# Performance work log

Hardware: AMD Instinct MI355X
Metric: run time of the kernel (lower is better)

## Reference

```python
import jax, jax.numpy as jnp
import numpy as np

IN_CH = 128
HIDDEN = 256
CHUNK = 4096
EPS = 1e-8  # F.cosine_similarity default eps


def setup_inputs() -> dict:
    key = jax.random.key(0)
    ks = jax.random.split(key, 10)
    N, E, P = 8192, 262144, 65536
    x = jax.random.normal(ks[0], (N, IN_CH), dtype=jnp.float32)
    edge_index = jax.random.randint(ks[1], (2, E), 0, N, dtype=jnp.int64)
    edge_pairs = jax.random.randint(ks[2], (P, 2), 0, N, dtype=jnp.int64)
    input_dim = 2 * IN_CH + IN_CH + IN_CH + IN_CH + 1 + 3  # 644
    h2 = HIDDEN // 2
    def lin(k, fan_in, fan_out):
        bound = 1.0 / np.sqrt(fan_in)
        kw, kb = jax.random.split(k)
        W = jax.random.uniform(kw, (fan_in, fan_out), minval=-bound, maxval=bound, dtype=jnp.float32)
        b = jax.random.uniform(kb, (fan_out,), minval=-bound, maxval=bound, dtype=jnp.float32)
        return W, b
    W1, b1 = lin(ks[3], input_dim, HIDDEN)
    W2, b2 = lin(ks[4], HIDDEN, h2)
    W3, b3 = lin(ks[5], h2, 1)
    return {"x": x, "edge_index": edge_index, "edge_pairs": edge_pairs,
            "W1": W1, "b1": b1, "W2": W2, "b2": b2, "W3": W3, "b3": b3}


def _forward(x, edge_index, edge_pairs, W1, b1, W2, b2, W3, b3):
    N = x.shape[0]
    # dense adjacency cache (matches DenseHeuristicMixin._ensure_graph_cache)
    adj = jnp.zeros((N, N), dtype=jnp.float32).at[edge_index[0], edge_index[1]].set(1.0)
    diag = jnp.arange(N)
    adj = adj.at[diag, diag].set(0.0)
    deg = adj.sum(axis=1)
    inv_log_deg = jnp.where(deg > 1, 1.0 / jnp.log(jnp.where(deg > 1, deg, 2.0)), 0.0)
    inv_deg = jnp.where(deg > 0, 1.0 / jnp.where(deg > 0, deg, 1.0), 0.0)

    P = edge_pairs.shape[0]
    pairs = edge_pairs.reshape(P // CHUNK, CHUNK, 2)

    def chunk_body(carry, pc):
        u, v = pc[:, 0], pc[:, 1]
        xu, xv = x[u], x[v]                          # [C, d]
        # cosine similarity (eps-clamped denominator, as in torch)
        nu = jnp.sqrt(jnp.sum(xu * xu, axis=1))
        nv = jnp.sqrt(jnp.sum(xv * xv, axis=1))
        cos = jnp.sum(xu * xv, axis=1) / jnp.maximum(nu * nv, EPS)
        # dense heuristic features: [C, N] adjacency-row products
        common = adj[u] * adj[v]
        cn = common.sum(axis=1)
        aa = common @ inv_log_deg
        ra = common @ inv_deg
        feats = jnp.concatenate(
            [xu, xv, xu * xv, jnp.abs(xu - xv), xu + xv,
             cos[:, None], cn[:, None], aa[:, None], ra[:, None]], axis=1)
        h = jax.nn.relu(feats @ W1 + b1)  # dropout is identity in eval mode
        h = jax.nn.relu(h @ W2 + b2)
        s = (h @ W3 + b3)[:, 0]
        return carry, s

    _, scores = jax.lax.scan(chunk_body, None, pairs)
    return scores.reshape(-1)


def reference(x, edge_index, edge_pairs, W1, b1, W2, b2, W3, b3):
    return _forward(x, edge_index, edge_pairs, W1, b1, W2, b2, W3, b3)
```

## Files before the change

kernel.cpp:

```cpp
#include <hip/hip_runtime.h>
#include <hip/hip_bf16.h>

#define IN_CH   128
#define HIDDEN  256
#define H2DIM   128
#define KS1     17
#define KS2     8
#define NT1     16
#define NT2     8
#define FSTRIDE 552
#define H1S     264
#define H2S     136
#define H2OFF   16896
#define CAP     64
#define T1PACK  (NT1*KS1*64)
#define T2PACK  (NT2*KS2*64)

typedef short short8v __attribute__((ext_vector_type(8)));
typedef float f32x4   __attribute__((ext_vector_type(4)));

__device__ __forceinline__ ushort f2bf(float f) {
  union { float f; uint32_t u; } c; c.f = f;
  uint32_t u = c.u + 0x7FFFu + ((c.u >> 16) & 1u);
  return (ushort)(u >> 16);
}
__device__ __forceinline__ float bf2f(ushort h) {
  union { uint32_t u; float f; } c; c.u = ((uint32_t)h) << 16;
  return c.f;
}
__device__ __forceinline__ uint32_t pk2(float a, float b) {
  __hip_bfloat162 h = __float22bfloat162_rn(make_float2(a, b));
  union { __hip_bfloat162 h; uint32_t u; } c; c.h = h;
  return c.u;
}
__device__ __forceinline__ uint4 pack8(float4 lo, float4 hi) {
  uint4 r;
  r.x = pk2(lo.x, lo.y); r.y = pk2(lo.z, lo.w);
  r.z = pk2(hi.x, hi.y); r.w = pk2(hi.z, hi.w);
  return r;
}

__global__ void k_prep(const float* __restrict__ W1, const float* __restrict__ W2,
                       ushort* __restrict__ w1p, ushort* __restrict__ w2p,
                       uint32_t* __restrict__ bits, int nwords) {
  int t = blockIdx.x * blockDim.x + threadIdx.x;
  if (t < T1PACK) {
    int l = t & 63;
    int rest = t >> 6;
    int ks = rest % KS1;
    int nt = rest / KS1;
    int n  = nt * 16 + (l & 15);
    int k0 = ks * 32 + (l >> 4) * 8;
    short8v v;
    #pragma unroll
    for (int j = 0; j < 8; ++j) {
      int k = k0 + j;
      float val;
      if (k < 128)      val = W1[(size_t)k * HIDDEN + n] + W1[(size_t)(512 + k) * HIDDEN + n];
      else if (k < 256) val = W1[(size_t)k * HIDDEN + n] + W1[(size_t)(384 + k) * HIDDEN + n];
      else if (k < 512) val = W1[(size_t)k * HIDDEN + n];
      else if (k < 516) val = W1[(size_t)(k + 128) * HIDDEN + n];
      else              val = 0.f;
      v[j] = (short)f2bf(val);
    }
    *(short8v*)(w1p + (size_t)t * 8) = v;
  } else if (t < T1PACK + T2PACK) {
    int t2 = t - T1PACK;
    int l = t2 & 63;
    int rest = t2 >> 6;
    int ks = rest % KS2;
    int nt = rest / KS2;
    int n  = nt * 16 + (l & 15);
    int k0 = ks * 32 + (l >> 4) * 8;
    short8v v;
    #pragma unroll
    for (int j = 0; j < 8; ++j)
      v[j] = (short)f2bf(W2[(size_t)(k0 + j) * H2DIM + n]);
    *(short8v*)(w2p + (size_t)t2 * 8) = v;
  }
  int stride = gridDim.x * blockDim.x;
  for (int i = t; i < nwords; i += stride) bits[i] = 0u;
}

__global__ void k_build_adj(const int* __restrict__ ei, int E, int roww,
                            uint32_t* __restrict__ bits) {
  int e = blockIdx.x * blockDim.x + threadIdx.x;
  if (e >= E) return;
  int u = ei[e];
  int v = ei[E + e];
  if (u == v) return;
  atomicOr((unsigned int*)&bits[(size_t)u * roww + (v >> 5)], 1u << (v & 31));
}

__global__ void k_node_lists(const uint32_t* __restrict__ bits, const float* __restrict__ x,
                             int nnodes, int roww,
                             float* __restrict__ invlog, float* __restrict__ invdeg,
                             int* __restrict__ deg, float* __restrict__ nrm,
                             ushort* __restrict__ adjl) {
  int node = blockIdx.x * (blockDim.x >> 6) + (threadIdx.x >> 6);
  int lane = threadIdx.x & 63;
  if (node >= nnodes) return;
  const uint32_t* row = bits + (size_t)node * roww;
  uint32_t wd[4];
  int c = 0;
  #pragma unroll
  for (int j = 0; j < 4; ++j) { wd[j] = row[lane * 4 + j]; c += __popc(wd[j]); }
  int sum = c;
  #pragma unroll
  for (int off = 1; off < 64; off <<= 1) {
    int t = __shfl_up(sum, off);
    if (lane >= off) sum += t;
  }
  int excl = sum - c;
  int total = __shfl(sum, 63);
  ushort* lst = adjl + (size_t)node * CAP;
  int pos = excl;
  #pragma unroll
  for (int j = 0; j < 4; ++j) {
    uint32_t m = wd[j];
    int base = (lane * 4 + j) * 32;
    while (m) {
      int b = __ffs(m) - 1;
      if (pos < CAP) lst[pos] = (ushort)(base + b);
      ++pos;
      m &= m - 1;
    }
  }
  float2 xa = *(const float2*)(x + (size_t)node * IN_CH + 2 * lane);
  float ss = xa.x * xa.x + xa.y * xa.y;
  #pragma unroll
  for (int off = 32; off; off >>= 1) ss += __shfl_xor(ss, off);
  if (lane == 0) {
    deg[node] = total;
    float d = (float)total;
    invlog[node] = (total > 1) ? 1.0f / logf(d) : 0.0f;
    invdeg[node] = (total > 0) ? 1.0f / d : 0.0f;
    nrm[node] = sqrtf(ss);
  }
}

__global__ __launch_bounds__(512, 4) void k_mlp4(
    const float* __restrict__ x, const int* __restrict__ pairs,
    const uint32_t* __restrict__ bits, int roww,
    const int* __restrict__ deg, const float* __restrict__ nrm,
    const float* __restrict__ invlog, const float* __restrict__ invdeg,
    const ushort* __restrict__ adjl,
    const ushort* __restrict__ w1p, const float* __restrict__ b1,
    const ushort* __restrict__ w2p, const float* __restrict__ b2,
    const float* __restrict__ W3, const float* __restrict__ b3,
    float* __restrict__ out, int P)
{
  __shared__ ushort feats[64 * FSTRIDE];
  __shared__ int us[64], vs[64];

  int tid = threadIdx.x;
  int pb = blockIdx.x * 64;
  int w  = tid >> 6, l = tid & 63;

  if (tid < 64) {
    int2 pr = ((const int2*)pairs)[pb + tid];
    us[tid] = pr.x; vs[tid] = pr.y;
  }
  __syncthreads();

  {
    int pg = l >> 3, g = l & 7;
    int p = w * 8 + pg;
    int u = us[p], v = vs[p];
    const float* xu = x + (size_t)u * IN_CH + g * 16;
    const float* xv = x + (size_t)v * IN_CH + g * 16;
    float4 a0 = *(const float4*)(xu + 0),  a1 = *(const float4*)(xu + 4);
    float4 a2 = *(const float4*)(xu + 8),  a3 = *(const float4*)(xu + 12);
    float4 b0 = *(const float4*)(xv + 0),  b1v = *(const float4*)(xv + 4);
    float4 b2v = *(const float4*)(xv + 8), b3v = *(const float4*)(xv + 12);
    ushort* fpR = feats + p * FSTRIDE;
    ushort* fp  = fpR + g * 16;
    *(uint4*)(fp)       = pack8(a0, a1);
    *(uint4*)(fp + 8)   = pack8(a2, a3);
    *(uint4*)(fp + 128) = pack8(b0, b1v);
    *(uint4*)(fp + 136) = pack8(b2v, b3v);
    float4 c0, c1, c2, c3, d0, d1, d2, d3;
    c0.x=a0.x*b0.x;  c0.y=a0.y*b0.y;  c0.z=a0.z*b0.z;  c0.w=a0.w*b0.w;
    c1.x=a1.x*b1v.x; c1.y=a1.y*b1v.y; c1.z=a1.z*b1v.z; c1.w=a1.w*b1v.w;
    c2.x=a2.x*b2v.x; c2.y=a2.y*b2v.y; c2.z=a2.z*b2v.z; c2.w=a2.w*b2v.w;
    c3.x=a3.x*b3v.x; c3.y=a3.y*b3v.y; c3.z=a3.z*b3v.z; c3.w=a3.w*b3v.w;
    d0.x=fabsf(a0.x-b0.x);  d0.y=fabsf(a0.y-b0.y);  d0.z=fabsf(a0.z-b0.z);  d0.w=fabsf(a0.w-b0.w);
    d1.x=fabsf(a1.x-b1v.x); d1.y=fabsf(a1.y-b1v.y); d1.z=fabsf(a1.z-b1v.z); d1.w=fabsf(a1.w-b1v.w);
    d2.x=fabsf(a2.x-b2v.x); d2.y=fabsf(a2.y-b2v.y); d2.z=fabsf(a2.z-b2v.z); d2.w=fabsf(a2.w-b2v.w);
    d3.x=fabsf(a3.x-b3v.x); d3.y=fabsf(a3.y-b3v.y); d3.z=fabsf(a3.z-b3v.z); d3.w=fabsf(a3.w-b3v.w);
    *(uint4*)(fp + 256) = pack8(c0, c1);
    *(uint4*)(fp + 264) = pack8(c2, c3);
    *(uint4*)(fp + 384) = pack8(d0, d1);
    *(uint4*)(fp + 392) = pack8(d2, d3);
    float suv = c0.x+c0.y+c0.z+c0.w + c1.x+c1.y+c1.z+c1.w
              + c2.x+c2.y+c2.z+c2.w + c3.x+c3.y+c3.z+c3.w;
    suv += __shfl_xor(suv, 1);
    suv += __shfl_xor(suv, 2);
    suv += __shfl_xor(suv, 4);
    if (g == 0) {
      float cosv = suv / fmaxf(nrm[u] * nrm[v], 1e-8f);
      fpR[512] = f2bf(cosv);
    }
    if (g < 7) {
      *(uint32_t*)(fpR + 516 + 4 * g) = 0u;
      *(uint32_t*)(fpR + 516 + 4 * g + 2) = 0u;
    }
  }

  for (int pp = 0; pp < 8; ++pp) {
    int p = w * 8 + pp;
    int u = us[p], v = vs[p];
    int du = deg[u], dv = deg[v];
    int s_ = (du <= dv) ? u : v;
    int o_ = (du <= dv) ? v : u;
    int dmin = min(du, dv);
    float cnv, aa = 0.f, ra = 0.f;
    if (dmin <= CAP) {
      bool h = false; int nb = 0;
      if (l < dmin) {
        nb = adjl[(size_t)s_ * CAP + l];
        h = (bits[(size_t)o_ * roww + (nb >> 5)] >> (nb & 31)) & 1u;
      }
      unsigned long long mask = __ballot(h);
      cnv = (float)__popcll(mask);
      if (mask) {
        float il = 0.f, ig = 0.f;
        if (h) { il = invlog[nb]; ig = invdeg[nb]; }
        while (mask) {
          int ln = __ffsll(mask) - 1;
          aa += __shfl(il, ln);
          ra += __shfl(ig, ln);
          mask &= mask - 1;
        }
      }
    } else {
      float cnL = 0.f, aaL = 0.f, raL = 0.f;
      const uint32_t* ru = bits + (size_t)u * roww;
      const uint32_t* rv = bits + (size_t)v * roww;
      for (int wd = l; wd < roww; wd += 64) {
        uint32_t c = ru[wd] & rv[wd];
        cnL += (float)__popc(c);
        while (c) {
          int bb = __ffs(c) - 1;
          int idx = wd * 32 + bb;
          aaL += invlog[idx]; raL += invdeg[idx];
          c &= c - 1;
        }
      }
      #pragma unroll
      for (int off = 32; off; off >>= 1) {
        cnL += __shfl_xor(cnL, off);
        aaL += __shfl_xor(aaL, off);
        raL += __shfl_xor(raL, off);
      }
      cnv = cnL; aa = aaL; ra = raL;
    }
    if (l == 0) {
      ushort* fpR = feats + p * FSTRIDE;
      fpR[513] = f2bf(cnv);
      fpR[514] = f2bf(aa);
      fpR[515] = f2bf(ra);
    }
  }
  __syncthreads();

  int lr = l & 15;
  int lk = l >> 4;

  f32x4 acc[4][2];
  #pragma unroll
  for (int m = 0; m < 4; ++m)
    #pragma unroll
    for (int i = 0; i < 2; ++i) acc[m][i] = (f32x4){0.f, 0.f, 0.f, 0.f};

  const ushort* aB = feats + lr * FSTRIDE + lk * 8;
  const ushort* bW = w1p + (size_t)(w * 2) * KS1 * 512 + l * 8;

  short8v bf[2][2];
  #pragma unroll
  for (int i = 0; i < 2; ++i)
    bf[0][i] = *(const short8v*)(bW + (size_t)(i * KS1) * 512);

  #pragma unroll
  for (int ks = 0; ks < KS1; ++ks) {
    int cur = ks & 1, nxt = cur ^ 1;
    if (ks + 1 < KS1) {
      #pragma unroll
      for (int i = 0; i < 2; ++i)
        bf[nxt][i] = *(const short8v*)(bW + (size_t)(i * KS1 + ks + 1) * 512);
    }
    short8v am[4];
    #pragma unroll
    for (int m = 0; m < 4; ++m)
      am[m] = *(const short8v*)(aB + m * 16 * FSTRIDE + ks * 32);
    #pragma unroll
    for (int i = 0; i < 2; ++i)
      #pragma unroll
      for (int m = 0; m < 4; ++m)
        acc[m][i] = __builtin_amdgcn_mfma_f32_16x16x32_bf16(am[m], bf[cur][i], acc[m][i], 0, 0, 0);
  }

  uint32_t h1r[2][8];
  #pragma unroll
  for (int i = 0; i < 2; ++i) {
    float bias = b1[(w * 2 + i) * 16 + lr];
    #pragma unroll
    for (int m = 0; m < 4; ++m) {
      float v0 = fmaxf(acc[m][i][0] + bias, 0.f);
      float v1 = fmaxf(acc[m][i][1] + bias, 0.f);
      float v2 = fmaxf(acc[m][i][2] + bias, 0.f);
      float v3 = fmaxf(acc[m][i][3] + bias, 0.f);
      h1r[i][m * 2]     = pk2(v0, v1);
      h1r[i][m * 2 + 1] = pk2(v2, v3);
    }
  }
  __syncthreads();

  ushort* h1 = feats;
  #pragma unroll
  for (int i = 0; i < 2; ++i) {
    int col = (w * 2 + i) * 16 + lr;
    #pragma unroll
    for (int m = 0; m < 4; ++m) {
      int row0 = m * 16 + lk * 4;
      h1[(row0)     * H1S + col] = (ushort)(h1r[i][m * 2]);
      h1[(row0 + 1) * H1S + col] = (ushort)(h1r[i][m * 2] >> 16);
      h1[(row0 + 2) * H1S + col] = (ushort)(h1r[i][m * 2 + 1]);
      h1[(row0 + 3) * H1S + col] = (ushort)(h1r[i][m * 2 + 1] >> 16);
    }
  }
  __syncthreads();

  f32x4 acc2[4];
  #pragma unroll
  for (int m = 0; m < 4; ++m) acc2[m] = (f32x4){0.f, 0.f, 0.f, 0.f};

  const ushort* aB2 = h1 + lr * H1S + lk * 8;
  const ushort* bW2 = w2p + (size_t)w * KS2 * 512 + l * 8;

  short8v b2f[2];
  b2f[0] = *(const short8v*)(bW2);

  #pragma unroll
  for (int ks = 0; ks < KS2; ++ks) {
    int cur = ks & 1, nxt = cur ^ 1;
    if (ks + 1 < KS2)
      b2f[nxt] = *(const short8v*)(bW2 + (size_t)(ks + 1) * 512);
    #pragma unroll
    for (int m = 0; m < 4; ++m) {
      short8v am = *(const short8v*)(aB2 + m * 16 * H1S + ks * 32);
      acc2[m] = __builtin_amdgcn_mfma_f32_16x16x32_bf16(am, b2f[cur], acc2[m], 0, 0, 0);
    }
  }

  ushort* h2 = feats + H2OFF;
  {
    int col = w * 16 + lr;
    float bias = b2[col];
    #pragma unroll
    for (int m = 0; m < 4; ++m) {
      int row0 = m * 16 + lk * 4;
      #pragma unroll
      for (int r = 0; r < 4; ++r)
        h2[(row0 + r) * H2S + col] = f2bf(fmaxf(acc2[m][r] + bias, 0.f));
    }
  }
  __syncthreads();

  {
    int p = tid >> 3, g = tid & 7;
    const ushort* hp = h2 + p * H2S + g * 16;
    float s = 0.f;
    #pragma unroll
    for (int j = 0; j < 16; ++j) s += bf2f(hp[j]) * W3[g * 16 + j];
    s += __shfl_down(s, 4, 8);
    s += __shfl_down(s, 2, 8);
    s += __shfl_down(s, 1, 8);
    if (g == 0) out[pb + p] = s + b3[0];
  }
}

extern "C" void kernel_launch(void* const* d_in, const int* in_sizes, int n_in,
                              void* d_out, int out_size, void* d_ws, size_t ws_size,
                              hipStream_t stream) {
  const float* x     = (const float*)d_in[0];
  const int*   ei    = (const int*)d_in[1];
  const int*   pairs = (const int*)d_in[2];
  const float* W1    = (const float*)d_in[3];
  const float* b1    = (const float*)d_in[4];
  const float* W2    = (const float*)d_in[5];
  const float* b2    = (const float*)d_in[6];
  const float* W3    = (const float*)d_in[7];
  const float* b3    = (const float*)d_in[8];
  float* out = (float*)d_out;

  int N = in_sizes[0] / IN_CH;
  int E = in_sizes[1] / 2;
  int P = in_sizes[2] / 2;
  int roww = (N + 31) >> 5;

  char* wsb = (char*)d_ws;
  uint32_t* bits = (uint32_t*)wsb;                       size_t off = (size_t)N * roww * 4;
  float* invlog  = (float*)(wsb + off);                  off += (size_t)N * 4;
  float* invdeg  = (float*)(wsb + off);                  off += (size_t)N * 4;
  int*   deg     = (int*)(wsb + off);                    off += (size_t)N * 4;
  float* nrm     = (float*)(wsb + off);                  off += (size_t)N * 4;
  ushort* adjl   = (ushort*)(wsb + off);                 off += (size_t)N * CAP * 2;
  ushort* w1pack = (ushort*)(wsb + off);                 off += (size_t)T1PACK * 8 * 2;
  ushort* w2pack = (ushort*)(wsb + off);                 off += (size_t)T2PACK * 8 * 2;

  int nwords = N * roww;
  k_prep<<<1024, 256, 0, stream>>>(W1, W2, w1pack, w2pack, bits, nwords);
  k_build_adj<<<(E + 255) / 256, 256, 0, stream>>>(ei, E, roww, bits);
  k_node_lists<<<(N + 3) / 4, 256, 0, stream>>>(bits, x, N, roww, invlog, invdeg, deg, nrm, adjl);
  k_mlp4<<<P / 64, 512, 0, stream>>>(x, pairs, bits, roww, deg, nrm, invlog, invdeg, adjl,
                                     w1pack, b1, w2pack, b2, W3, b3, out, P);
}
```

Baseline: 81.33 us.

## Merge graph-prep kernels into cooperative kernel and batch heuristic loads

The prep, adjacency-build and node-list kernels become one cooperative kernel that separates its phases with grid-wide syncs, which removes two kernel launches and their gaps. In the MLP kernel, each wave now loads the pair indices, degrees, neighbour-list entries and adjacency bit words for all eight of its pairs before the common-neighbour computation, so these dependent global loads can overlap instead of running one pair at a time. The cost is extra registers per thread and grid.sync overhead, plus an all-or-nothing fallback to the slow bitmap path when any of a wave's eight pairs exceeds the list cap. Neighbour-list entries are also read regardless of degree, and the index is masked with 8191.

```diff
diff --git a/kernel.cpp b/kernel.cpp
--- a/kernel.cpp
+++ b/kernel.cpp
@@ -1,5 +1,8 @@
 #include <hip/hip_runtime.h>
 #include <hip/hip_bf16.h>
+#include <hip/hip_cooperative_groups.h>
+
+namespace cg = cooperative_groups;
 
 #define IN_CH   128
 #define HIDDEN  256
@@ -40,10 +43,20 @@
   return r;
 }
 
-__global__ void k_prep(const float* __restrict__ W1, const float* __restrict__ W2,
-                       ushort* __restrict__ w1p, ushort* __restrict__ w2p,
-                       uint32_t* __restrict__ bits, int nwords) {
+__global__ void k_graph(const float* __restrict__ x, const int* __restrict__ ei,
+                        const float* __restrict__ W1, const float* __restrict__ W2,
+                        ushort* __restrict__ w1p, ushort* __restrict__ w2p,
+                        uint32_t* __restrict__ bits,
+                        float* __restrict__ invlog, float* __restrict__ invdeg,
+                        int* __restrict__ deg, float* __restrict__ nrm,
+                        ushort* __restrict__ adjl,
+                        int N, int E, int roww, int nwords) {
+  cg::grid_group grid = cg::this_grid();
   int t = blockIdx.x * blockDim.x + threadIdx.x;
+  int nthr = gridDim.x * blockDim.x;
+
+  for (int i = t; i < nwords; i += nthr) bits[i] = 0u;
+
   if (t < T1PACK) {
     int l = t & 63;
     int rest = t >> 6;
@@ -78,68 +91,61 @@
       v[j] = (short)f2bf(W2[(size_t)(k0 + j) * H2DIM + n]);
     *(short8v*)(w2p + (size_t)t2 * 8) = v;
   }
-  int stride = gridDim.x * blockDim.x;
-  for (int i = t; i < nwords; i += stride) bits[i] = 0u;
-}
-
-__global__ void k_build_adj(const int* __restrict__ ei, int E, int roww,
-                            uint32_t* __restrict__ bits) {
-  int e = blockIdx.x * blockDim.x + threadIdx.x;
-  if (e >= E) return;
-  int u = ei[e];
-  int v = ei[E + e];
-  if (u == v) return;
-  atomicOr((unsigned int*)&bits[(size_t)u * roww + (v >> 5)], 1u << (v & 31));
-}
-
-__global__ void k_node_lists(const uint32_t* __restrict__ bits, const float* __restrict__ x,
-                             int nnodes, int roww,
-                             float* __restrict__ invlog, float* __restrict__ invdeg,
-                             int* __restrict__ deg, float* __restrict__ nrm,
-                             ushort* __restrict__ adjl) {
-  int node = blockIdx.x * (blockDim.x >> 6) + (threadIdx.x >> 6);
-  int lane = threadIdx.x & 63;
-  if (node >= nnodes) return;
-  const uint32_t* row = bits + (size_t)node * roww;
-  uint32_t wd[4];
-  int c = 0;
-  #pragma unroll
-  for (int j = 0; j < 4; ++j) { wd[j] = row[lane * 4 + j]; c += __popc(wd[j]); }
-  int sum = c;
-  #pragma unroll
-  for (int off = 1; off < 64; off <<= 1) {
-    int t = __shfl_up(sum, off);
-    if (lane >= off) sum += t;
-  }
-  int excl = sum - c;
-  int total = __shfl(sum, 63);
-  ushort* lst = adjl + (size_t)node * CAP;
-  int pos = excl;
-  #pragma unroll
-  for (int j = 0; j < 4; ++j) {
-    uint32_t m = wd[j];
-    int base = (lane * 4 + j) * 32;
-    while (m) {
-      int b = __ffs(m) - 1;
-      if (pos < CAP) lst[pos] = (ushort)(base + b);
-      ++pos;
-      m &= m - 1;
-    }
-  }
-  float2 xa = *(const float2*)(x + (size_t)node * IN_CH + 2 * lane);
-  float ss = xa.x * xa.x + xa.y * xa.y;
-  #pragma unroll
-  for (int off = 32; off; off >>= 1) ss += __shfl_xor(ss, off);
-  if (lane == 0) {
-    deg[node] = total;
-    float d = (float)total;
-    invlog[node] = (total > 1) ? 1.0f / logf(d) : 0.0f;
-    invdeg[node] = (total > 0) ? 1.0f / d : 0.0f;
-    nrm[node] = sqrtf(ss);
-  }
-}
-
-__global__ __launch_bounds__(512, 4) void k_mlp4(
+
+  grid.sync();
+
+  for (int e = t; e < E; e += nthr) {
+    int u = ei[e];
+    int v = ei[E + e];
+    if (u != v)
+      atomicOr((unsigned int*)&bits[(size_t)u * roww + (v >> 5)], 1u << (v & 31));
+  }
+
+  grid.sync();
+
+  int wid = t >> 6, lane = t & 63, nwaves = nthr >> 6;
+  for (int node = wid; node < N; node += nwaves) {
+    const uint32_t* row = bits + (size_t)node * roww;
+    uint32_t wd[4];
+    int c = 0;
+    #pragma unroll
+    for (int j = 0; j < 4; ++j) { wd[j] = row[lane * 4 + j]; c += __popc(wd[j]); }
+    int sum = c;
+    #pragma unroll
+    for (int off = 1; off < 64; off <<= 1) {
+      int tt = __shfl_up(sum, off);
+      if (lane >= off) sum += tt;
+    }
+    int excl = sum - c;
+    int total = __shfl(sum, 63);
+    ushort* lst = adjl + (size_t)node * CAP;
+    int pos = excl;
+    #pragma unroll
+    for (int j = 0; j < 4; ++j) {
+      uint32_t m = wd[j];
+      int base = (lane * 4 + j) * 32;
+      while (m) {
+        int b = __ffs(m) - 1;
+        if (pos < CAP) lst[pos] = (ushort)(base + b);
+        ++pos;
+        m &= m - 1;
+      }
+    }
+    float2 xa = *(const float2*)(x + (size_t)node * IN_CH + 2 * lane);
+    float ss = xa.x * xa.x + xa.y * xa.y;
+    #pragma unroll
+    for (int off = 32; off; off >>= 1) ss += __shfl_xor(ss, off);
+    if (lane == 0) {
+      deg[node] = total;
+      float d = (float)total;
+      invlog[node] = (total > 1) ? 1.0f / logf(d) : 0.0f;
+      invdeg[node] = (total > 0) ? 1.0f / d : 0.0f;
+      nrm[node] = sqrtf(ss);
+    }
+  }
+}
+
+__global__ __launch_bounds__(512, 4) void k_mlp5(
     const float* __restrict__ x, const int* __restrict__ pairs,
     const uint32_t* __restrict__ bits, int roww,
     const int* __restrict__ deg, const float* __restrict__ nrm,
@@ -162,6 +168,19 @@
     us[tid] = pr.x; vs[tid] = pr.y;
   }
   __syncthreads();
+
+  int pu[8], pv[8];
+  #pragma unroll
+  for (int pp = 0; pp < 8; ++pp) { pu[pp] = us[w * 8 + pp]; pv[pp] = vs[w * 8 + pp]; }
+  int du[8], dv[8];
+  #pragma unroll
+  for (int pp = 0; pp < 8; ++pp) { du[pp] = deg[pu[pp]]; dv[pp] = deg[pv[pp]]; }
+  int nbu[8], nbv[8];
+  #pragma unroll
+  for (int pp = 0; pp < 8; ++pp) {
+    nbu[pp] = adjl[(size_t)pu[pp] * CAP + l];
+    nbv[pp] = adjl[(size_t)pv[pp] * CAP + l];
+  }
 
   {
     int pg = l >> 3, g = l & 7;
@@ -207,59 +226,73 @@
     }
   }
 
-  for (int pp = 0; pp < 8; ++pp) {
-    int p = w * 8 + pp;
-    int u = us[p], v = vs[p];
-    int du = deg[u], dv = deg[v];
-    int s_ = (du <= dv) ? u : v;
-    int o_ = (du <= dv) ? v : u;
-    int dmin = min(du, dv);
-    float cnv, aa = 0.f, ra = 0.f;
-    if (dmin <= CAP) {
-      bool h = false; int nb = 0;
-      if (l < dmin) {
-        nb = adjl[(size_t)s_ * CAP + l];
-        h = (bits[(size_t)o_ * roww + (nb >> 5)] >> (nb & 31)) & 1u;
-      }
-      unsigned long long mask = __ballot(h);
-      cnv = (float)__popcll(mask);
-      if (mask) {
-        float il = 0.f, ig = 0.f;
-        if (h) { il = invlog[nb]; ig = invdeg[nb]; }
-        while (mask) {
-          int ln = __ffsll(mask) - 1;
-          aa += __shfl(il, ln);
-          ra += __shfl(ig, ln);
-          mask &= mask - 1;
+  {
+    int dmin[8], nbs[8];
+    uint32_t wrd[8];
+    bool fall = false;
+    #pragma unroll
+    for (int pp = 0; pp < 8; ++pp) {
+      bool ule = du[pp] <= dv[pp];
+      dmin[pp] = ule ? du[pp] : dv[pp];
+      int o   = ule ? pv[pp] : pu[pp];
+      int nb  = (ule ? nbu[pp] : nbv[pp]) & 8191;
+      nbs[pp] = nb;
+      wrd[pp] = bits[(size_t)o * roww + (nb >> 5)];
+      fall |= (dmin[pp] > CAP);
+    }
+    if (!fall) {
+      #pragma unroll
+      for (int pp = 0; pp < 8; ++pp) {
+        bool h = (l < dmin[pp]) && ((wrd[pp] >> (nbs[pp] & 31)) & 1u);
+        unsigned long long mask = __ballot(h);
+        float cnv = (float)__popcll(mask);
+        float aa = 0.f, ra = 0.f;
+        if (mask) {
+          float il = 0.f, ig = 0.f;
+          if (h) { il = invlog[nbs[pp]]; ig = invdeg[nbs[pp]]; }
+          while (mask) {
+            int ln = __ffsll(mask) - 1;
+            aa += __shfl(il, ln);
+            ra += __shfl(ig, ln);
+            mask &= mask - 1;
+          }
+        }
+        if (l == 0) {
+          ushort* fpR = feats + (w * 8 + pp) * FSTRIDE;
+          fpR[513] = f2bf(cnv);
+          fpR[514] = f2bf(aa);
+          fpR[515] = f2bf(ra);
         }
       }
     } else {
-      float cnL = 0.f, aaL = 0.f, raL = 0.f;
-      const uint32_t* ru = bits + (size_t)u * roww;
-      const uint32_t* rv = bits + (size_t)v * roww;
-      for (int wd = l; wd < roww; wd += 64) {
-        uint32_t c = ru[wd] & rv[wd];
-        cnL += (float)__popc(c);
-        while (c) {
-          int bb = __ffs(c) - 1;
-          int idx = wd * 32 + bb;
-          aaL += invlog[idx]; raL += invdeg[idx];
-          c &= c - 1;
+      for (int pp = 0; pp < 8; ++pp) {
+        int u = pu[pp], v = pv[pp];
+        float cnL = 0.f, aaL = 0.f, raL = 0.f;
+        const uint32_t* ru = bits + (size_t)u * roww;
+        const uint32_t* rv = bits + (size_t)v * roww;
+        for (int wd = l; wd < roww; wd += 64) {
+          uint32_t c = ru[wd] & rv[wd];
+          cnL += (float)__popc(c);
+          while (c) {
+            int bb = __ffs(c) - 1;
+            int idx = wd * 32 + bb;
+            aaL += invlog[idx]; raL += invdeg[idx];
+            c &= c - 1;
+          }
+        }
+        #pragma unroll
+        for (int off = 32; off; off >>= 1) {
+          cnL += __shfl_xor(cnL, off);
+          aaL += __shfl_xor(aaL, off);
+          raL += __shfl_xor(raL, off);
+        }
+        if (l == 0) {
+          ushort* fpR = feats + (w * 8 + pp) * FSTRIDE;
+          fpR[513] = f2bf(cnL);
+          fpR[514] = f2bf(aaL);
+          fpR[515] = f2bf(raL);
         }
       }
-      #pragma unroll
-      for (int off = 32; off; off >>= 1) {
-        cnL += __shfl_xor(cnL, off);
-        aaL += __shfl_xor(aaL, off);
-        raL += __shfl_xor(raL, off);
-      }
-      cnv = cnL; aa = aaL; ra = raL;
-    }
-    if (l == 0) {
-      ushort* fpR = feats + p * FSTRIDE;
-      fpR[513] = f2bf(cnv);
-      fpR[514] = f2bf(aa);
-      fpR[515] = f2bf(ra);
     }
   }
   __syncthreads();
@@ -410,9 +443,11 @@
   ushort* w2pack = (ushort*)(wsb + off);                 off += (size_t)T2PACK * 8 * 2;
 
   int nwords = N * roww;
-  k_prep<<<1024, 256, 0, stream>>>(W1, W2, w1pack, w2pack, bits, nwords);
-  k_build_adj<<<(E + 255) / 256, 256, 0, stream>>>(ei, E, roww, bits);
-  k_node_lists<<<(N + 3) / 4, 256, 0, stream>>>(bits, x, N, roww, invlog, invdeg, deg, nrm, adjl);
-  k_mlp4<<<P / 64, 512, 0, stream>>>(x, pairs, bits, roww, deg, nrm, invlog, invdeg, adjl,
+  void* gargs[] = { (void*)&x, (void*)&ei, (void*)&W1, (void*)&W2,
+                    (void*)&w1pack, (void*)&w2pack, (void*)&bits,
+                    (void*)&invlog, (void*)&invdeg, (void*)&deg, (void*)&nrm,
+                    (void*)&adjl, (void*)&N, (void*)&E, (void*)&roww, (void*)&nwords };
+  hipLaunchCooperativeKernel((void*)k_graph, dim3(1024), dim3(256), gargs, 0, stream);
+  k_mlp5<<<P / 64, 512, 0, stream>>>(x, pairs, bits, roww, deg, nrm, invlog, invdeg, adjl,
                                      w1pack, b1, w2pack, b2, W3, b3, out, P);
 }
```

Result: slower. 253.7 us (+212.0%).

## Halve feature LDS tile by splitting GEMM1 K into two passes, batch neighbor loads

Applied to the files above, without the earlier changes.

Shrinks the per-block shared feature buffer to about half by computing the first layer's K dimension in two passes. The first pass covers xu, xv, cos and the heuristics. Then xu*xv and |xu-xv| are recomputed from re-read x rows into the same buffer for the second pass. This is meant to let more blocks reside per CU (launch bounds raised to 8). Common-neighbor loads for all 8 pairs per wave are now issued up front to overlap latency. The final W3 dot product is fused into the layer-2 epilogue via shuffles and LDS atomics, removing the h2 staging buffer. The cost is extra global reads of x, additional barriers, and register pressure under the tighter occupancy bound.

```diff
diff --git a/kernel.cpp b/kernel.cpp
--- a/kernel.cpp
+++ b/kernel.cpp
@@ -8,10 +8,8 @@
 #define KS2     8
 #define NT1     16
 #define NT2     8
-#define FSTRIDE 552
+#define FSTR    296
 #define H1S     264
-#define H2S     136
-#define H2OFF   16896
 #define CAP     64
 #define T1PACK  (NT1*KS1*64)
 #define T2PACK  (NT2*KS2*64)
@@ -139,7 +137,7 @@
   }
 }
 
-__global__ __launch_bounds__(512, 4) void k_mlp4(
+__global__ __launch_bounds__(512, 8) void k_mlp7(
     const float* __restrict__ x, const int* __restrict__ pairs,
     const uint32_t* __restrict__ bits, int roww,
     const int* __restrict__ deg, const float* __restrict__ nrm,
@@ -150,35 +148,164 @@
     const float* __restrict__ W3, const float* __restrict__ b3,
     float* __restrict__ out, int P)
 {
-  __shared__ ushort feats[64 * FSTRIDE];
+  __shared__ ushort feats[64 * FSTR];
+  __shared__ float outacc[64];
   __shared__ int us[64], vs[64];
 
   int tid = threadIdx.x;
   int pb = blockIdx.x * 64;
   int w  = tid >> 6, l = tid & 63;
+  int pg = l >> 3, g = l & 7;
+  int lr = l & 15;
+  int lk = l >> 4;
 
   if (tid < 64) {
     int2 pr = ((const int2*)pairs)[pb + tid];
     us[tid] = pr.x; vs[tid] = pr.y;
-  }
-  __syncthreads();
-
-  {
-    int pg = l >> 3, g = l & 7;
-    int p = w * 8 + pg;
-    int u = us[p], v = vs[p];
-    const float* xu = x + (size_t)u * IN_CH + g * 16;
-    const float* xv = x + (size_t)v * IN_CH + g * 16;
+    outacc[tid] = b3[0];
+  }
+  __syncthreads();
+
+  int p = w * 8 + pg;
+  int u = us[p], v = vs[p];
+  const float* xu = x + (size_t)u * IN_CH + g * 16;
+  const float* xv = x + (size_t)v * IN_CH + g * 16;
+  ushort* fpR = feats + p * FSTR;
+  ushort* fp  = fpR + g * 16;
+
+  {
     float4 a0 = *(const float4*)(xu + 0),  a1 = *(const float4*)(xu + 4);
     float4 a2 = *(const float4*)(xu + 8),  a3 = *(const float4*)(xu + 12);
     float4 b0 = *(const float4*)(xv + 0),  b1v = *(const float4*)(xv + 4);
     float4 b2v = *(const float4*)(xv + 8), b3v = *(const float4*)(xv + 12);
-    ushort* fpR = feats + p * FSTRIDE;
-    ushort* fp  = fpR + g * 16;
     *(uint4*)(fp)       = pack8(a0, a1);
     *(uint4*)(fp + 8)   = pack8(a2, a3);
     *(uint4*)(fp + 128) = pack8(b0, b1v);
     *(uint4*)(fp + 136) = pack8(b2v, b3v);
+    float suv = a0.x*b0.x + a0.y*b0.y + a0.z*b0.z + a0.w*b0.w
+              + a1.x*b1v.x + a1.y*b1v.y + a1.z*b1v.z + a1.w*b1v.w
+              + a2.x*b2v.x + a2.y*b2v.y + a2.z*b2v.z + a2.w*b2v.w
+              + a3.x*b3v.x + a3.y*b3v.y + a3.z*b3v.z + a3.w*b3v.w;
+    suv += __shfl_xor(suv, 1);
+    suv += __shfl_xor(suv, 2);
+    suv += __shfl_xor(suv, 4);
+    if (g == 0) fpR[256] = f2bf(suv / fmaxf(nrm[u] * nrm[v], 1e-8f));
+    if (g < 7) *(uint2*)(fpR + 260 + 4 * g) = make_uint2(0u, 0u);
+  }
+
+  {
+    int sdmin[8], snbs[8];
+    uint32_t swrd[8];
+    bool sfall = false;
+    #pragma unroll
+    for (int pp = 0; pp < 8; ++pp) {
+      int ps_ = w * 8 + pp;
+      int uu = us[ps_], vv = vs[ps_];
+      int du = deg[uu], dv = deg[vv];
+      int nu = adjl[(size_t)uu * CAP + l];
+      int nv = adjl[(size_t)vv * CAP + l];
+      bool ule = du <= dv;
+      sdmin[pp] = ule ? du : dv;
+      int o  = ule ? vv : uu;
+      int nb = (ule ? nu : nv) & 8191;
+      snbs[pp] = nb;
+      swrd[pp] = bits[(size_t)o * roww + (nb >> 5)];
+      sfall |= (sdmin[pp] > CAP);
+    }
+    if (!sfall) {
+      #pragma unroll
+      for (int pp = 0; pp < 8; ++pp) {
+        bool h = (l < sdmin[pp]) && ((swrd[pp] >> (snbs[pp] & 31)) & 1u);
+        unsigned long long mask = __ballot(h);
+        float cnv = (float)__popcll(mask);
+        float aa = 0.f, ra = 0.f;
+        if (mask) {
+          float il = 0.f, ig = 0.f;
+          if (h) { il = invlog[snbs[pp]]; ig = invdeg[snbs[pp]]; }
+          while (mask) {
+            int ln = __ffsll(mask) - 1;
+            aa += __shfl(il, ln);
+            ra += __shfl(ig, ln);
+            mask &= mask - 1;
+          }
+        }
+        if (l == 0) {
+          ushort* fq = feats + (w * 8 + pp) * FSTR;
+          fq[257] = f2bf(cnv); fq[258] = f2bf(aa); fq[259] = f2bf(ra);
+        }
+      }
+    } else {
+      for (int pp = 0; pp < 8; ++pp) {
+        int ps_ = w * 8 + pp;
+        int uu = us[ps_], vv = vs[ps_];
+        float cnL = 0.f, aaL = 0.f, raL = 0.f;
+        const uint32_t* ru = bits + (size_t)uu * roww;
+        const uint32_t* rv = bits + (size_t)vv * roww;
+        for (int wd = l; wd < roww; wd += 64) {
+          uint32_t c = ru[wd] & rv[wd];
+          cnL += (float)__popc(c);
+          while (c) {
+            int bb = __ffs(c) - 1;
+            int idx = wd * 32 + bb;
+            aaL += invlog[idx]; raL += invdeg[idx];
+            c &= c - 1;
+          }
+        }
+        #pragma unroll
+        for (int off = 32; off; off >>= 1) {
+          cnL += __shfl_xor(cnL, off);
+          aaL += __shfl_xor(aaL, off);
+          raL += __shfl_xor(raL, off);
+        }
+        if (l == 0) {
+          ushort* fq = feats + (w * 8 + pp) * FSTR;
+          fq[257] = f2bf(cnL); fq[258] = f2bf(aaL); fq[259] = f2bf(raL);
+        }
+      }
+    }
+  }
+  __syncthreads();
+
+  f32x4 acc[4][2];
+  #pragma unroll
+  for (int m = 0; m < 4; ++m)
+    #pragma unroll
+    for (int i = 0; i < 2; ++i) acc[m][i] = (f32x4){0.f, 0.f, 0.f, 0.f};
+
+  const ushort* aB = feats + lr * FSTR + lk * 8;
+  const ushort* bW = w1p + (size_t)(w * 2) * KS1 * 512 + l * 8;
+
+  {
+    short8v bf[2][2];
+    #pragma unroll
+    for (int i = 0; i < 2; ++i)
+      bf[0][i] = *(const short8v*)(bW + (size_t)(i * KS1) * 512);
+    #pragma unroll
+    for (int ks = 0; ks < 8; ++ks) {
+      int cur = ks & 1, nxt = cur ^ 1;
+      if (ks + 1 < 8) {
+        #pragma unroll
+        for (int i = 0; i < 2; ++i)
+          bf[nxt][i] = *(const short8v*)(bW + (size_t)(i * KS1 + ks + 1) * 512);
+      }
+      short8v am[4];
+      #pragma unroll
+      for (int m = 0; m < 4; ++m)
+        am[m] = *(const short8v*)(aB + m * 16 * FSTR + ks * 32);
+      #pragma unroll
+      for (int i = 0; i < 2; ++i)
+        #pragma unroll
+        for (int m = 0; m < 4; ++m)
+          acc[m][i] = __builtin_amdgcn_mfma_f32_16x16x32_bf16(am[m], bf[cur][i], acc[m][i], 0, 0, 0);
+    }
+  }
+  __syncthreads();
+
+  {
+    float4 a0 = *(const float4*)(xu + 0),  a1 = *(const float4*)(xu + 4);
+    float4 a2 = *(const float4*)(xu + 8),  a3 = *(const float4*)(xu + 12);
+    float4 b0 = *(const float4*)(xv + 0),  b1v = *(const float4*)(xv + 4);
+    float4 b2v = *(const float4*)(xv + 8), b3v = *(const float4*)(xv + 12);
     float4 c0, c1, c2, c3, d0, d1, d2, d3;
     c0.x=a0.x*b0.x;  c0.y=a0.y*b0.y;  c0.z=a0.z*b0.z;  c0.w=a0.w*b0.w;
     c1.x=a1.x*b1v.x; c1.y=a1.y*b1v.y; c1.z=a1.z*b1v.z; c1.w=a1.w*b1v.w;
@@ -188,116 +315,36 @@
     d1.x=fabsf(a1.x-b1v.x); d1.y=fabsf(a1.y-b1v.y); d1.z=fabsf(a1.z-b1v.z); d1.w=fabsf(a1.w-b1v.w);
     d2.x=fabsf(a2.x-b2v.x); d2.y=fabsf(a2.y-b2v.y); d2.z=fabsf(a2.z-b2v.z); d2.w=fabsf(a2.w-b2v.w);
     d3.x=fabsf(a3.x-b3v.x); d3.y=fabsf(a3.y-b3v.y); d3.z=fabsf(a3.z-b3v.z); d3.w=fabsf(a3.w-b3v.w);
-    *(uint4*)(fp + 256) = pack8(c0, c1);
-    *(uint4*)(fp + 264) = pack8(c2, c3);
-    *(uint4*)(fp + 384) = pack8(d0, d1);
-    *(uint4*)(fp + 392) = pack8(d2, d3);
-    float suv = c0.x+c0.y+c0.z+c0.w + c1.x+c1.y+c1.z+c1.w
-              + c2.x+c2.y+c2.z+c2.w + c3.x+c3.y+c3.z+c3.w;
-    suv += __shfl_xor(suv, 1);
-    suv += __shfl_xor(suv, 2);
-    suv += __shfl_xor(suv, 4);
-    if (g == 0) {
-      float cosv = suv / fmaxf(nrm[u] * nrm[v], 1e-8f);
-      fpR[512] = f2bf(cosv);
-    }
-    if (g < 7) {
-      *(uint32_t*)(fpR + 516 + 4 * g) = 0u;
-      *(uint32_t*)(fpR + 516 + 4 * g + 2) = 0u;
-    }
-  }
-
-  for (int pp = 0; pp < 8; ++pp) {
-    int p = w * 8 + pp;
-    int u = us[p], v = vs[p];
-    int du = deg[u], dv = deg[v];
-    int s_ = (du <= dv) ? u : v;
-    int o_ = (du <= dv) ? v : u;
-    int dmin = min(du, dv);
-    float cnv, aa = 0.f, ra = 0.f;
-    if (dmin <= CAP) {
-      bool h = false; int nb = 0;
-      if (l < dmin) {
-        nb = adjl[(size_t)s_ * CAP + l];
-        h = (bits[(size_t)o_ * roww + (nb >> 5)] >> (nb & 31)) & 1u;
+    *(uint4*)(fp)       = pack8(c0, c1);
+    *(uint4*)(fp + 8)   = pack8(c2, c3);
+    *(uint4*)(fp + 128) = pack8(d0, d1);
+    *(uint4*)(fp + 136) = pack8(d2, d3);
+  }
+  __syncthreads();
+
+  {
+    short8v bf[2][2];
+    #pragma unroll
+    for (int i = 0; i < 2; ++i)
+      bf[0][i] = *(const short8v*)(bW + (size_t)(i * KS1 + 8) * 512);
+    #pragma unroll
+    for (int ks = 8; ks < KS1; ++ks) {
+      int cur = ks & 1, nxt = cur ^ 1;
+      if (ks + 1 < KS1) {
+        #pragma unroll
+        for (int i = 0; i < 2; ++i)
+          bf[nxt][i] = *(const short8v*)(bW + (size_t)(i * KS1 + ks + 1) * 512);
       }
-      unsigned long long mask = __ballot(h);
-      cnv = (float)__popcll(mask);
-      if (mask) {
-        float il = 0.f, ig = 0.f;
-        if (h) { il = invlog[nb]; ig = invdeg[nb]; }
-        while (mask) {
-          int ln = __ffsll(mask) - 1;
-          aa += __shfl(il, ln);
-          ra += __shfl(ig, ln);
-          mask &= mask - 1;
-        }
-      }
-    } else {
-      float cnL = 0.f, aaL = 0.f, raL = 0.f;
-      const uint32_t* ru = bits + (size_t)u * roww;
-      const uint32_t* rv = bits + (size_t)v * roww;
-      for (int wd = l; wd < roww; wd += 64) {
-        uint32_t c = ru[wd] & rv[wd];
-        cnL += (float)__popc(c);
-        while (c) {
-          int bb = __ffs(c) - 1;
-          int idx = wd * 32 + bb;
-          aaL += invlog[idx]; raL += invdeg[idx];
-          c &= c - 1;
-        }
-      }
-      #pragma unroll
-      for (int off = 32; off; off >>= 1) {
-        cnL += __shfl_xor(cnL, off);
-        aaL += __shfl_xor(aaL, off);
-        raL += __shfl_xor(raL, off);
-      }
-      cnv = cnL; aa = aaL; ra = raL;
-    }
-    if (l == 0) {
-      ushort* fpR = feats + p * FSTRIDE;
-      fpR[513] = f2bf(cnv);
-      fpR[514] = f2bf(aa);
-      fpR[515] = f2bf(ra);
-    }
-  }
-  __syncthreads();
-
-  int lr = l & 15;
-  int lk = l >> 4;
-
-  f32x4 acc[4][2];
-  #pragma unroll
-  for (int m = 0; m < 4; ++m)
-    #pragma unroll
-    for (int i = 0; i < 2; ++i) acc[m][i] = (f32x4){0.f, 0.f, 0.f, 0.f};
-
-  const ushort* aB = feats + lr * FSTRIDE + lk * 8;
-  const ushort* bW = w1p + (size_t)(w * 2) * KS1 * 512 + l * 8;
-
-  short8v bf[2][2];
-  #pragma unroll
-  for (int i = 0; i < 2; ++i)
-    bf[0][i] = *(const short8v*)(bW + (size_t)(i * KS1) * 512);
-
-  #pragma unroll
-  for (int ks = 0; ks < KS1; ++ks) {
-    int cur = ks & 1, nxt = cur ^ 1;
-    if (ks + 1 < KS1) {
+      short8v am[4];
+      #pragma unroll
+      for (int m = 0; m < 4; ++m)
+        am[m] = *(const short8v*)(aB + m * 16 * FSTR + (ks - 8) * 32);
       #pragma unroll
       for (int i = 0; i < 2; ++i)
-        bf[nxt][i] = *(const short8v*)(bW + (size_t)(i * KS1 + ks + 1) * 512);
-    }
-    short8v am[4];
-    #pragma unroll
-    for (int m = 0; m < 4; ++m)
-      am[m] = *(const short8v*)(aB + m * 16 * FSTRIDE + ks * 32);
-    #pragma unroll
-    for (int i = 0; i < 2; ++i)
-      #pragma unroll
-      for (int m = 0; m < 4; ++m)
-        acc[m][i] = __builtin_amdgcn_mfma_f32_16x16x32_bf16(am[m], bf[cur][i], acc[m][i], 0, 0, 0);
+        #pragma unroll
+        for (int m = 0; m < 4; ++m)
+          acc[m][i] = __builtin_amdgcn_mfma_f32_16x16x32_bf16(am[m], bf[cur][i], acc[m][i], 0, 0, 0);
+    }
   }
 
   uint32_t h1r[2][8];
@@ -353,31 +400,26 @@
     }
   }
 
-  ushort* h2 = feats + H2OFF;
   {
     int col = w * 16 + lr;
     float bias = b2[col];
+    float w3v = W3[col];
     #pragma unroll
     for (int m = 0; m < 4; ++m) {
-      int row0 = m * 16 + lk * 4;
-      #pragma unroll
-      for (int r = 0; r < 4; ++r)
-        h2[(row0 + r) * H2S + col] = f2bf(fmaxf(acc2[m][r] + bias, 0.f));
-    }
-  }
-  __syncthreads();
-
-  {
-    int p = tid >> 3, g = tid & 7;
-    const ushort* hp = h2 + p * H2S + g * 16;
-    float s = 0.f;
-    #pragma unroll
-    for (int j = 0; j < 16; ++j) s += bf2f(hp[j]) * W3[g * 16 + j];
-    s += __shfl_down(s, 4, 8);
-    s += __shfl_down(s, 2, 8);
-    s += __shfl_down(s, 1, 8);
-    if (g == 0) out[pb + p] = s + b3[0];
-  }
+      #pragma unroll
+      for (int r = 0; r < 4; ++r) {
+        float h = fmaxf(acc2[m][r] + bias, 0.f) * w3v;
+        h += __shfl_xor(h, 1);
+        h += __shfl_xor(h, 2);
+        h += __shfl_xor(h, 4);
+        h += __shfl_xor(h, 8);
+        if (lr == 0) atomicAdd(&outacc[m * 16 + lk * 4 + r], h);
+      }
+    }
+  }
+  __syncthreads();
+
+  if (tid < 64) out[pb + tid] = outacc[tid];
 }
 
 extern "C" void kernel_launch(void* const* d_in, const int* in_sizes, int n_in,
@@ -413,6 +455,6 @@
   k_prep<<<1024, 256, 0, stream>>>(W1, W2, w1pack, w2pack, bits, nwords);
   k_build_adj<<<(E + 255) / 256, 256, 0, stream>>>(ei, E, roww, bits);
   k_node_lists<<<(N + 3) / 4, 256, 0, stream>>>(bits, x, N, roww, invlog, invdeg, deg, nrm, adjl);
-  k_mlp4<<<P / 64, 512, 0, stream>>>(x, pairs, bits, roww, deg, nrm, invlog, invdeg, adjl,
+  k_mlp7<<<P / 64, 512, 0, stream>>>(x, pairs, bits, roww, deg, nrm, invlog, invdeg, adjl,
                                      w1pack, b1, w2pack, b2, W3, b3, out, P);
 }
```

Measured after the change: 108.2 us. +33.0%, slower.
